# Kernel optimization log

Measured on AMD Instinct MI355X. Metric: run time of the kernel, lower is better.

## Reference

```python
import jax, jax.numpy as jnp
import numpy as np

N = 8192
F_IN = 128
D = 128
NEG_SLOPE = 0.2  # cfg.negativeslope (standard GAT value)
MASK_FILL = -9e15


def setup_inputs() -> dict:
    key = jax.random.key(0)
    k1, k2, k3, k4 = jax.random.split(key, 4)
    A = jax.random.randint(k1, (N, N), 0, 2, dtype=jnp.int32)
    X = jax.random.normal(k2, (N, F_IN), dtype=jnp.float32)
    # glorot init for Ws, xavier_uniform(gain=1.414) for a
    lim_w = float(np.sqrt(6.0 / (F_IN + D)))
    Ws = jax.random.uniform(k3, (F_IN, D), minval=-lim_w, maxval=lim_w, dtype=jnp.float32)
    lim_a = 1.414 * float(np.sqrt(6.0 / (2 * D + 1)))
    a = jax.random.uniform(k4, (2 * D, 1), minval=-lim_a, maxval=lim_a, dtype=jnp.float32)
    return {"A": A, "X": X, "Ws": Ws, "a": a}


def reference(A, X, Ws, a):
    # Wh: [N, D]
    Wh = X @ Ws
    d = Wh.shape[-1]
    # additive attention: e_ij = leaky_relu(Wh_i . a1 + Wh_j . a2)
    e1 = Wh @ a[:d]          # [N, 1]
    e2 = Wh @ a[d:]          # [N, 1]
    e = jax.nn.leaky_relu(e1 + e2.T, negative_slope=NEG_SLOPE)  # [N, N]
    e = jnp.where(A > 0, e, MASK_FILL)
    attn = jax.nn.softmax(e, axis=1)  # row-wise over neighbors
    H = attn @ Wh            # [N, D]
    return H
```

## Files before the change

### kernel.cpp

```cpp
#include <hip/hip_runtime.h>
#include <hip/hip_bf16.h>

#define NN 8192
#define DD 128

typedef __attribute__((ext_vector_type(8))) short short8;
typedef __attribute__((ext_vector_type(4))) float f32x4;
typedef __attribute__((ext_vector_type(4))) int i32x4;
typedef unsigned int u32;

__device__ __forceinline__ ushort f2bf(float f) {
    __hip_bfloat16 h = __float2bfloat16(f);
    return *(ushort*)&h;
}

__device__ __forceinline__ void async_ld16(const void* g, void* l) {
    __builtin_amdgcn_global_load_lds(
        (const __attribute__((address_space(1))) u32*)g,
        (__attribute__((address_space(3))) u32*)l, 16, 0, 0);
}

__global__ __launch_bounds__(256) void k12_gemm(const float* __restrict__ X,
                                                const float* __restrict__ Ws,
                                                const float* __restrict__ a,
                                                ushort* __restrict__ WhT,
                                                float* __restrict__ C1,
                                                float* __restrict__ C1s,
                                                float2* __restrict__ E2) {
    __shared__ float lWs[128 * 132];
    __shared__ float lX[32 * 132];
    __shared__ ushort lT2[128 * 32];
    __shared__ float la[256];
    int t = threadIdx.x, bx = blockIdx.x;
    la[t] = a[t];
    const float4* Ws4 = (const float4*)Ws;
    const float4* X4 = (const float4*)X;
    for (int j = 0; j < 16; ++j) {
        int u = j * 256 + t;
        int k = u >> 5, c4 = u & 31;
        *(float4*)&lWs[k * 132 + c4 * 4] = Ws4[u];
    }
    for (int j = 0; j < 4; ++j) {
        int u = j * 256 + t;
        int r = u >> 5, c4 = u & 31;
        *(float4*)&lX[r * 132 + c4 * 4] = X4[bx * 1024 + u];
    }
    __syncthreads();
    int r0 = (t >> 5) * 4, c0 = (t & 31) * 4;
    float acc[4][4];
#pragma unroll
    for (int i = 0; i < 4; ++i)
#pragma unroll
        for (int j = 0; j < 4; ++j) acc[i][j] = 0.f;
#pragma unroll 4
    for (int k = 0; k < 128; ++k) {
        float4 wv = *(const float4*)&lWs[k * 132 + c0];
        float x0 = lX[(r0 + 0) * 132 + k];
        float x1 = lX[(r0 + 1) * 132 + k];
        float x2 = lX[(r0 + 2) * 132 + k];
        float x3 = lX[(r0 + 3) * 132 + k];
#pragma unroll
        for (int j = 0; j < 4; ++j) {
            acc[0][j] += x0 * ((const float*)&wv)[j];
            acc[1][j] += x1 * ((const float*)&wv)[j];
            acc[2][j] += x2 * ((const float*)&wv)[j];
            acc[3][j] += x3 * ((const float*)&wv)[j];
        }
    }
#pragma unroll
    for (int i = 0; i < 4; ++i)
#pragma unroll
        for (int j = 0; j < 4; ++j)
            lT2[(c0 + j) * 32 + r0 + i] = f2bf(acc[i][j]);
    float p1[4], p2[4];
#pragma unroll
    for (int i = 0; i < 4; ++i) {
        p1[i] = 0.f; p2[i] = 0.f;
#pragma unroll
        for (int j = 0; j < 4; ++j) {
            p1[i] += acc[i][j] * la[c0 + j];
            p2[i] += acc[i][j] * la[128 + c0 + j];
        }
    }
#pragma unroll
    for (int m = 1; m < 32; m <<= 1) {
#pragma unroll
        for (int i = 0; i < 4; ++i) {
            p1[i] += __shfl_xor(p1[i], m);
            p2[i] += __shfl_xor(p2[i], m);
        }
    }
    if ((t & 31) == 0) {
#pragma unroll
        for (int i = 0; i < 4; ++i) {
            int row = bx * 32 + r0 + i;
            C1[row]  = __expf(p1[i]);
            C1s[row] = __expf(0.2f * p1[i]);
            E2[row]  = make_float2(__expf(p2[i]), __expf(0.2f * p2[i]));
        }
    }
    __syncthreads();
    {
        int d = t >> 1, hf = t & 1;
        uint4* dst = (uint4*)&WhT[(size_t)d * NN + bx * 32 + hf * 16];
        const uint4* src = (const uint4*)&lT2[d * 32 + hf * 16];
        dst[0] = src[0];
        dst[1] = src[1];
    }
}

#define PACK4(b, v, sh)                                     \
    b |= (u32)((v).x & 1) << (sh);                          \
    b |= (u32)((v).y & 1) << ((sh) + 1);                    \
    b |= (u32)((v).z & 1) << ((sh) + 2);                    \
    b |= (u32)((v).w & 1) << ((sh) + 3);

__global__ __launch_bounds__(256, 2) void k3_main(
    const int* __restrict__ A, const ushort* __restrict__ WhT,
    const float* __restrict__ C1, const float* __restrict__ C1s,
    const float2* __restrict__ E2,
    float* __restrict__ Hp, float* __restrict__ Lp) {

    __shared__ __align__(16) char lB[2 * 32768];
    __shared__ __align__(16) char lE[2 * 1024];

    int tid = threadIdx.x;
    int lane = tid & 63;
    int w = tid >> 6;
    int n = lane & 15;
    int kg = lane >> 4;

    int bx = blockIdx.x;
    int kb = blockIdx.y;
    int rb = bx * 128 + w * 32;
    int kt0 = kb * 8;

    float c1_0 = C1[rb + n],      c1s_0 = C1s[rb + n];
    float c1_1 = C1[rb + 16 + n], c1s_1 = C1s[rb + 16 + n];

    const char* srcB[8];
    char* dstB[8];
#pragma unroll
    for (int i = 0; i < 8; ++i) {
        srcB[i] = (const char*)(WhT + (size_t)(i * 16 + n) * NN +
                                (size_t)kt0 * 128 + w * 32 + kg * 8);
        dstB[i] = lB + (w * 8 + i) * 1024 + lane * 16;
    }
    const char* srcE = (const char*)(E2 + (size_t)kt0 * 128) + lane * 16;

    const int* pA0 = A + (size_t)(rb + n) * NN + kb * 1024 + kg * 8;
    const int* pA1 = pA0 + (size_t)16 * NN;

    i32x4 ar[16];
    u32 a_cur0, a_cur1;

#pragma unroll
    for (int tp = 0; tp < 4; ++tp) {
        ar[tp * 2 + 0]     = __builtin_nontemporal_load((const i32x4*)(pA0 + tp * 32));
        ar[tp * 2 + 1]     = __builtin_nontemporal_load((const i32x4*)(pA0 + tp * 32 + 4));
        ar[8 + tp * 2 + 0] = __builtin_nontemporal_load((const i32x4*)(pA1 + tp * 32));
        ar[8 + tp * 2 + 1] = __builtin_nontemporal_load((const i32x4*)(pA1 + tp * 32 + 4));
    }
#pragma unroll
    for (int i = 0; i < 8; ++i) async_ld16(srcB[i], dstB[i]);
    if (w == 0) async_ld16(srcE, lE + lane * 16);
    {
        u32 b0 = 0, b1 = 0;
#pragma unroll
        for (int tp = 0; tp < 4; ++tp) {
            PACK4(b0, ar[tp * 2 + 0], tp * 8);
            PACK4(b0, ar[tp * 2 + 1], tp * 8 + 4);
            PACK4(b1, ar[8 + tp * 2 + 0], tp * 8);
            PACK4(b1, ar[8 + tp * 2 + 1], tp * 8 + 4);
        }
        a_cur0 = b0; a_cur1 = b1;
    }

    short8 ones;
#pragma unroll
    for (int j = 0; j < 8; ++j) ones[j] = (short)0x3F80;

    f32x4 acc0[8], acc1[8];
#pragma unroll
    for (int c = 0; c < 8; ++c) {
        acc0[c] = (f32x4){0.f, 0.f, 0.f, 0.f};
        acc1[c] = (f32x4){0.f, 0.f, 0.f, 0.f};
    }
    f32x4 accl0 = (f32x4){0.f, 0.f, 0.f, 0.f};
    f32x4 accl1 = (f32x4){0.f, 0.f, 0.f, 0.f};

    __syncthreads();

    for (int kt = 0; kt < 8; ++kt) {
        int buf = kt & 1;
        if (kt < 7) {
#pragma unroll
            for (int tp = 0; tp < 4; ++tp) {
                ar[tp * 2 + 0]     = __builtin_nontemporal_load((const i32x4*)(pA0 + (kt + 1) * 128 + tp * 32));
                ar[tp * 2 + 1]     = __builtin_nontemporal_load((const i32x4*)(pA0 + (kt + 1) * 128 + tp * 32 + 4));
                ar[8 + tp * 2 + 0] = __builtin_nontemporal_load((const i32x4*)(pA1 + (kt + 1) * 128 + tp * 32));
                ar[8 + tp * 2 + 1] = __builtin_nontemporal_load((const i32x4*)(pA1 + (kt + 1) * 128 + tp * 32 + 4));
            }
            int bo = (buf ^ 1) * 32768;
#pragma unroll
            for (int i = 0; i < 8; ++i)
                async_ld16(srcB[i] + (kt + 1) * 256, dstB[i] + bo);
            if (w == 0)
                async_ld16(srcE + (kt + 1) * 1024, lE + (buf ^ 1) * 1024 + lane * 16);
        }
        const char* bB = lB + buf * 32768;
        const float* bE = (const float*)(lE + buf * 1024);
#pragma unroll
        for (int tp = 0; tp < 4; ++tp) {
            const float4* ev = (const float4*)(bE + (tp * 32 + kg * 8) * 2);
            float pe[16];
            *(float4*)(pe + 0)  = ev[0];
            *(float4*)(pe + 4)  = ev[1];
            *(float4*)(pe + 8)  = ev[2];
            *(float4*)(pe + 12) = ev[3];
            u32 ab0 = (a_cur0 >> (tp * 8)) & 0xffu;
            u32 ab1 = (a_cur1 >> (tp * 8)) & 0xffu;
            short8 af0, af1;
#pragma unroll
            for (int u = 0; u < 8; ++u) {
                float w0 = fmaxf(c1_0 * pe[2 * u], c1s_0 * pe[2 * u + 1]);
                float w1 = fmaxf(c1_1 * pe[2 * u], c1s_1 * pe[2 * u + 1]);
                af0[u] = ((ab0 >> u) & 1u) ? (short)f2bf(w0) : (short)0;
                af1[u] = ((ab1 >> u) & 1u) ? (short)f2bf(w1) : (short)0;
            }
            const short8* bb = (const short8*)(bB + tp * 8192);
#pragma unroll
            for (int c = 0; c < 8; ++c) {
                short8 bf = bb[c * 64 + lane];
                acc0[c] = __builtin_amdgcn_mfma_f32_16x16x32_bf16(af0, bf, acc0[c], 0, 0, 0);
                acc1[c] = __builtin_amdgcn_mfma_f32_16x16x32_bf16(af1, bf, acc1[c], 0, 0, 0);
            }
            accl0 = __builtin_amdgcn_mfma_f32_16x16x32_bf16(af0, ones, accl0, 0, 0, 0);
            accl1 = __builtin_amdgcn_mfma_f32_16x16x32_bf16(af1, ones, accl1, 0, 0, 0);
        }
        if (kt < 7) {
            u32 b0 = 0, b1 = 0;
#pragma unroll
            for (int tp = 0; tp < 4; ++tp) {
                PACK4(b0, ar[tp * 2 + 0], tp * 8);
                PACK4(b0, ar[tp * 2 + 1], tp * 8 + 4);
                PACK4(b1, ar[8 + tp * 2 + 0], tp * 8);
                PACK4(b1, ar[8 + tp * 2 + 1], tp * 8 + 4);
            }
            a_cur0 = b0; a_cur1 = b1;
        }
        __syncthreads();
    }

    float* Hpb = Hp + (size_t)kb * (NN * DD);
#pragma unroll
    for (int c = 0; c < 8; ++c)
#pragma unroll
        for (int r = 0; r < 4; ++r) {
            Hpb[(size_t)(rb + kg * 4 + r) * DD + c * 16 + n]      = acc0[c][r];
            Hpb[(size_t)(rb + 16 + kg * 4 + r) * DD + c * 16 + n] = acc1[c][r];
        }
    if (n == 0) {
        float* Lpb = Lp + (size_t)kb * NN;
#pragma unroll
        for (int r = 0; r < 4; ++r) {
            Lpb[rb + kg * 4 + r]      = accl0[r];
            Lpb[rb + 16 + kg * 4 + r] = accl1[r];
        }
    }
}

__global__ void k4_final(const float* __restrict__ Hp, const float* __restrict__ Lp,
                         float* __restrict__ out) {
    int idx = blockIdx.x * 256 + threadIdx.x;
    int i = idx >> 7;
    float sv = 0.f, l = 0.f;
#pragma unroll
    for (int kb = 0; kb < 8; ++kb) {
        sv += Hp[(size_t)kb * (NN * DD) + idx];
        l  += Lp[(size_t)kb * NN + i];
    }
    out[idx] = sv / l;
}

extern "C" void kernel_launch(void* const* d_in, const int* in_sizes, int n_in,
                              void* d_out, int out_size, void* d_ws, size_t ws_size,
                              hipStream_t stream) {
    const int*   A  = (const int*)d_in[0];
    const float* X  = (const float*)d_in[1];
    const float* Ws = (const float*)d_in[2];
    const float* a  = (const float*)d_in[3];
    float* out = (float*)d_out;

    char* ws = (char*)d_ws;
    ushort* WhT = (ushort*)(ws);
    float*  C1  = (float*)(ws + (2u << 20));
    float*  C1s = (float*)(ws + (2u << 20) + (32u << 10));
    float2* E2  = (float2*)(ws + (2u << 20) + (64u << 10));
    float*  Hp  = (float*)(ws + (3u << 20));
    float*  Lp  = (float*)(ws + (35u << 20));

    k12_gemm<<<256, 256, 0, stream>>>(X, Ws, a, WhT, C1, C1s, E2);
    k3_main<<<dim3(64, 8), 256, 0, stream>>>(A, WhT, C1, C1s, E2, Hp, Lp);
    k4_final<<<4096, 256, 0, stream>>>(Hp, Lp, out);
}
```

Baseline: 424.0 us.

## Split K dimension into 16 chunks with smaller tiles and vectorized reduction

The main attention-aggregation kernel now splits the neighbor dimension into 16 slices instead of 8. It uses half-size K tiles (64 columns per step) and half the LDS buffer, and raises the occupancy hint to 3 blocks per CU, so twice as many blocks run with more resident waves to hide the latency of streaming A. The E2 coefficient buffer is loaded once every two steps. The final reduction kernel sums 16 partials and is vectorized to float4 with a reciprocal multiply. In exchange, partial-result traffic doubles (Hp grows to 64 MB), which makes the reduction kernel more expensive.

```diff
diff --git a/kernel.cpp b/kernel.cpp
--- a/kernel.cpp
+++ b/kernel.cpp
@@ -115,13 +115,13 @@
     b |= (u32)((v).z & 1) << ((sh) + 2);                    \
     b |= (u32)((v).w & 1) << ((sh) + 3);
 
-__global__ __launch_bounds__(256, 2) void k3_main(
+__global__ __launch_bounds__(256, 3) void k3_main(
     const int* __restrict__ A, const ushort* __restrict__ WhT,
     const float* __restrict__ C1, const float* __restrict__ C1s,
     const float2* __restrict__ E2,
     float* __restrict__ Hp, float* __restrict__ Lp) {
 
-    __shared__ __align__(16) char lB[2 * 32768];
+    __shared__ __align__(16) char lB[2 * 16384];
     __shared__ __align__(16) char lE[2 * 1024];
 
     int tid = threadIdx.x;
@@ -133,45 +133,46 @@
     int bx = blockIdx.x;
     int kb = blockIdx.y;
     int rb = bx * 128 + w * 32;
-    int kt0 = kb * 8;
 
     float c1_0 = C1[rb + n],      c1s_0 = C1s[rb + n];
     float c1_1 = C1[rb + 16 + n], c1s_1 = C1s[rb + 16 + n];
 
-    const char* srcB[8];
-    char* dstB[8];
-#pragma unroll
-    for (int i = 0; i < 8; ++i) {
-        srcB[i] = (const char*)(WhT + (size_t)(i * 16 + n) * NN +
-                                (size_t)kt0 * 128 + w * 32 + kg * 8);
-        dstB[i] = lB + (w * 8 + i) * 1024 + lane * 16;
-    }
-    const char* srcE = (const char*)(E2 + (size_t)kt0 * 128) + lane * 16;
-
-    const int* pA0 = A + (size_t)(rb + n) * NN + kb * 1024 + kg * 8;
+    const char* srcB[4];
+    char* dstB[4];
+#pragma unroll
+    for (int i = 0; i < 4; ++i) {
+        int p = 4 * w + i;
+        int c = p & 7, tp = p >> 3;
+        srcB[i] = (const char*)(WhT + (size_t)(c * 16 + n) * NN +
+                                (size_t)kb * 512 + tp * 32 + kg * 8);
+        dstB[i] = lB + p * 1024 + lane * 16;
+    }
+    const char* srcE = (const char*)(E2 + (size_t)kb * 512) + lane * 16;
+
+    const int* pA0 = A + (size_t)(rb + n) * NN + (size_t)kb * 512 + kg * 8;
     const int* pA1 = pA0 + (size_t)16 * NN;
 
-    i32x4 ar[16];
+    i32x4 ar[8];
     u32 a_cur0, a_cur1;
 
 #pragma unroll
-    for (int tp = 0; tp < 4; ++tp) {
+    for (int tp = 0; tp < 2; ++tp) {
         ar[tp * 2 + 0]     = __builtin_nontemporal_load((const i32x4*)(pA0 + tp * 32));
         ar[tp * 2 + 1]     = __builtin_nontemporal_load((const i32x4*)(pA0 + tp * 32 + 4));
-        ar[8 + tp * 2 + 0] = __builtin_nontemporal_load((const i32x4*)(pA1 + tp * 32));
-        ar[8 + tp * 2 + 1] = __builtin_nontemporal_load((const i32x4*)(pA1 + tp * 32 + 4));
-    }
-#pragma unroll
-    for (int i = 0; i < 8; ++i) async_ld16(srcB[i], dstB[i]);
+        ar[4 + tp * 2 + 0] = __builtin_nontemporal_load((const i32x4*)(pA1 + tp * 32));
+        ar[4 + tp * 2 + 1] = __builtin_nontemporal_load((const i32x4*)(pA1 + tp * 32 + 4));
+    }
+#pragma unroll
+    for (int i = 0; i < 4; ++i) async_ld16(srcB[i], dstB[i]);
     if (w == 0) async_ld16(srcE, lE + lane * 16);
     {
         u32 b0 = 0, b1 = 0;
 #pragma unroll
-        for (int tp = 0; tp < 4; ++tp) {
+        for (int tp = 0; tp < 2; ++tp) {
             PACK4(b0, ar[tp * 2 + 0], tp * 8);
             PACK4(b0, ar[tp * 2 + 1], tp * 8 + 4);
-            PACK4(b1, ar[8 + tp * 2 + 0], tp * 8);
-            PACK4(b1, ar[8 + tp * 2 + 1], tp * 8 + 4);
+            PACK4(b1, ar[4 + tp * 2 + 0], tp * 8);
+            PACK4(b1, ar[4 + tp * 2 + 1], tp * 8 + 4);
         }
         a_cur0 = b0; a_cur1 = b1;
     }
@@ -195,23 +196,25 @@
         int buf = kt & 1;
         if (kt < 7) {
 #pragma unroll
-            for (int tp = 0; tp < 4; ++tp) {
-                ar[tp * 2 + 0]     = __builtin_nontemporal_load((const i32x4*)(pA0 + (kt + 1) * 128 + tp * 32));
-                ar[tp * 2 + 1]     = __builtin_nontemporal_load((const i32x4*)(pA0 + (kt + 1) * 128 + tp * 32 + 4));
-                ar[8 + tp * 2 + 0] = __builtin_nontemporal_load((const i32x4*)(pA1 + (kt + 1) * 128 + tp * 32));
-                ar[8 + tp * 2 + 1] = __builtin_nontemporal_load((const i32x4*)(pA1 + (kt + 1) * 128 + tp * 32 + 4));
+            for (int tp = 0; tp < 2; ++tp) {
+                ar[tp * 2 + 0]     = __builtin_nontemporal_load((const i32x4*)(pA0 + (kt + 1) * 64 + tp * 32));
+                ar[tp * 2 + 1]     = __builtin_nontemporal_load((const i32x4*)(pA0 + (kt + 1) * 64 + tp * 32 + 4));
+                ar[4 + tp * 2 + 0] = __builtin_nontemporal_load((const i32x4*)(pA1 + (kt + 1) * 64 + tp * 32));
+                ar[4 + tp * 2 + 1] = __builtin_nontemporal_load((const i32x4*)(pA1 + (kt + 1) * 64 + tp * 32 + 4));
             }
-            int bo = (buf ^ 1) * 32768;
-#pragma unroll
-            for (int i = 0; i < 8; ++i)
-                async_ld16(srcB[i] + (kt + 1) * 256, dstB[i] + bo);
-            if (w == 0)
-                async_ld16(srcE + (kt + 1) * 1024, lE + (buf ^ 1) * 1024 + lane * 16);
-        }
-        const char* bB = lB + buf * 32768;
-        const float* bE = (const float*)(lE + buf * 1024);
-#pragma unroll
-        for (int tp = 0; tp < 4; ++tp) {
+            int bo = (buf ^ 1) * 16384;
+#pragma unroll
+            for (int i = 0; i < 4; ++i)
+                async_ld16(srcB[i] + (kt + 1) * 128, dstB[i] + bo);
+        }
+        if (w == 1 && (kt & 1) == 0 && kt < 6)
+            async_ld16(srcE + (kt / 2 + 1) * 1024,
+                       lE + (((kt >> 1) + 1) & 1) * 1024 + lane * 16);
+
+        const char* bB = lB + buf * 16384;
+        const float* bE = (const float*)(lE + ((kt >> 1) & 1) * 1024) + (kt & 1) * 128;
+#pragma unroll
+        for (int tp = 0; tp < 2; ++tp) {
             const float4* ev = (const float4*)(bE + (tp * 32 + kg * 8) * 2);
             float pe[16];
             *(float4*)(pe + 0)  = ev[0];
@@ -241,11 +244,11 @@
         if (kt < 7) {
             u32 b0 = 0, b1 = 0;
 #pragma unroll
-            for (int tp = 0; tp < 4; ++tp) {
+            for (int tp = 0; tp < 2; ++tp) {
                 PACK4(b0, ar[tp * 2 + 0], tp * 8);
                 PACK4(b0, ar[tp * 2 + 1], tp * 8 + 4);
-                PACK4(b1, ar[8 + tp * 2 + 0], tp * 8);
-                PACK4(b1, ar[8 + tp * 2 + 1], tp * 8 + 4);
+                PACK4(b1, ar[4 + tp * 2 + 0], tp * 8);
+                PACK4(b1, ar[4 + tp * 2 + 1], tp * 8 + 4);
             }
             a_cur0 = b0; a_cur1 = b1;
         }
@@ -272,15 +275,18 @@
 
 __global__ void k4_final(const float* __restrict__ Hp, const float* __restrict__ Lp,
                          float* __restrict__ out) {
-    int idx = blockIdx.x * 256 + threadIdx.x;
-    int i = idx >> 7;
-    float sv = 0.f, l = 0.f;
-#pragma unroll
-    for (int kb = 0; kb < 8; ++kb) {
-        sv += Hp[(size_t)kb * (NN * DD) + idx];
-        l  += Lp[(size_t)kb * NN + i];
-    }
-    out[idx] = sv / l;
+    int g = blockIdx.x * 256 + threadIdx.x;
+    int i = g >> 5;
+    float4 sv = make_float4(0.f, 0.f, 0.f, 0.f);
+    float l = 0.f;
+#pragma unroll
+    for (int kb = 0; kb < 16; ++kb) {
+        float4 v = *(const float4*)(Hp + (size_t)kb * (NN * DD) + (size_t)g * 4);
+        sv.x += v.x; sv.y += v.y; sv.z += v.z; sv.w += v.w;
+        l += Lp[(size_t)kb * NN + i];
+    }
+    float r = 1.f / l;
+    *(float4*)(out + (size_t)g * 4) = make_float4(sv.x * r, sv.y * r, sv.z * r, sv.w * r);
 }
 
 extern "C" void kernel_launch(void* const* d_in, const int* in_sizes, int n_in,
@@ -298,9 +304,9 @@
     float*  C1s = (float*)(ws + (2u << 20) + (32u << 10));
     float2* E2  = (float2*)(ws + (2u << 20) + (64u << 10));
     float*  Hp  = (float*)(ws + (3u << 20));
-    float*  Lp  = (float*)(ws + (35u << 20));
+    float*  Lp  = (float*)(ws + (67u << 20));
 
     k12_gemm<<<256, 256, 0, stream>>>(X, Ws, a, WhT, C1, C1s, E2);
-    k3_main<<<dim3(64, 8), 256, 0, stream>>>(A, WhT, C1, C1s, E2, Hp, Lp);
-    k4_final<<<4096, 256, 0, stream>>>(Hp, Lp, out);
-}
+    k3_main<<<dim3(64, 16), 256, 0, stream>>>(A, WhT, C1, C1s, E2, Hp, Lp);
+    k4_final<<<1024, 256, 0, stream>>>(Hp, Lp, out);
+}
```

Measured after the change: 407.8 us. 1.04x faster.
